# Kernel tuning notes

Measured on AMD Instinct MI355X. Metric: run time of the kernel, lower is better.

The kernel has to match this reference:

```python
import jax, jax.numpy as jnp
import numpy as np

B, CIN, COUT, KH, KW = 8, 64, 128, 3, 3
H = W = 64
STRIDE, PAD = 1, 1
G = 1  # deformable groups


def setup_inputs() -> dict:
    key = jax.random.key(0)
    k1, k2, k3 = jax.random.split(key, 3)
    rgb = jax.random.normal(k1, (B, CIN, H, W), dtype=jnp.float32)
    # torchvision layout: [B, 2*G*KH*KW, Ho, Wo], (dy, dx) pairs per kernel tap
    offsets = jax.random.normal(k2, (B, 2 * G * KH * KW, H, W), dtype=jnp.float32)
    # xavier_uniform for weight [COUT, CIN, KH, KW]
    fan_in, fan_out = CIN * KH * KW, COUT * KH * KW
    a = float(np.sqrt(6.0 / (fan_in + fan_out)))
    weight = jax.random.uniform(k3, (COUT, CIN, KH, KW), dtype=jnp.float32, minval=-a, maxval=a)
    bias = jnp.zeros((COUT,), dtype=jnp.float32)
    return {"rgb": rgb, "offsets": offsets, "weight": weight, "bias": bias}


def _deform_conv2d(rgb, offsets, weight, bias):
    b, cin, h, w = rgb.shape
    cout, _, kh, kw = weight.shape
    K = kh * kw
    ho = (h + 2 * PAD - kh) // STRIDE + 1
    wo = (w + 2 * PAD - kw) // STRIDE + 1
    cg = cin // G  # channels per deformable group

    off = offsets.reshape(b, G, K, 2, ho, wo)
    dy, dx = off[:, :, :, 0], off[:, :, :, 1]  # [b, G, K, ho, wo]

    ky, kx = jnp.meshgrid(jnp.arange(kh), jnp.arange(kw), indexing="ij")
    ky = ky.reshape(K).astype(jnp.float32)
    kx = kx.reshape(K).astype(jnp.float32)
    base_y = (jnp.arange(ho) * STRIDE - PAD).astype(jnp.float32)
    base_x = (jnp.arange(wo) * STRIDE - PAD).astype(jnp.float32)

    # sampling coordinates: p0 + kernel tap + learned offset -> [b, G, K, ho, wo]
    y = base_y[None, None, None, :, None] + ky[None, None, :, None, None] + dy
    x = base_x[None, None, None, None, :] + kx[None, None, :, None, None] + dx

    y0 = jnp.floor(y)
    x0 = jnp.floor(x)
    fy = y - y0
    fx = x - x0
    y0i = y0.astype(jnp.int32)
    x0i = x0.astype(jnp.int32)

    x_flat = rgb.reshape(b, G, cg, h * w)
    P = K * ho * wo

    def gather_corner(yc, xc, wgt):
        valid = (yc >= 0) & (yc < h) & (xc >= 0) & (xc < w)
        idx = jnp.clip(yc, 0, h - 1) * w + jnp.clip(xc, 0, w - 1)
        wgt = jnp.where(valid, wgt, 0.0).reshape(b, G, 1, P)
        vals = jnp.take_along_axis(x_flat, idx.reshape(b, G, 1, P), axis=3)
        return vals * wgt

    col = (
        gather_corner(y0i, x0i, (1 - fy) * (1 - fx))
        + gather_corner(y0i, x0i + 1, (1 - fy) * fx)
        + gather_corner(y0i + 1, x0i, fy * (1 - fx))
        + gather_corner(y0i + 1, x0i + 1, fy * fx)
    )  # [b, G, cg, K*ho*wo]

    col = col.reshape(b, cin * K, ho * wo)
    out = jnp.einsum("ok,bkp->bop", weight.reshape(cout, cin * K), col)
    return out.reshape(b, cout, ho, wo) + bias[None, :, None, None]


def reference(rgb, offsets, weight, bias):
    return _deform_conv2d(rgb, offsets, weight, bias)
```

## Files before the change

### kernel.cpp

```cpp
#include <hip/hip_runtime.h>

#define COUT_  128
#define KP     1024
#define CAPR   20
#define IMGC   (21 * 64)
#define IMGBUF (4 * IMGC)
#define COLU   36
#define COLBUF (64 * COLU)
#define WS_NEED (size_t)(COUT_ * KP * 2 + 8ull * 64 * 64 * 64 * 4)

#if __has_builtin(__builtin_amdgcn_fdot2_f32_bf16)
#define HAS_DOT2 1
#else
#define HAS_DOT2 0
#endif

typedef __attribute__((ext_vector_type(8))) __bf16 bf16x8;
typedef __attribute__((ext_vector_type(2))) __bf16 bf16x2;
typedef unsigned short u16x8 __attribute__((ext_vector_type(8)));
typedef __attribute__((ext_vector_type(4))) float f32x4;

__device__ __forceinline__ unsigned int f2bf(float f) {
    union { float f; unsigned int u; } c; c.f = f;
    unsigned int u = c.u;
    u += 0x7fffu + ((u >> 16) & 1u);
    return u >> 16;
}
__device__ __forceinline__ float bitsf(unsigned int u) {
    union { unsigned int u; float f; } c; c.u = u; return c.f;
}
__device__ __forceinline__ unsigned int pk2bf(float lo, float hi) {
    return f2bf(lo) | (f2bf(hi) << 16);
}
__device__ __forceinline__ bf16x2 mk_bf2(float lo, float hi) {
    unsigned int u = pk2bf(lo, hi);
    return __builtin_bit_cast(bf16x2, u);
}
__device__ __forceinline__ void gl_lds16(const unsigned int* g, unsigned int* l) {
    __builtin_amdgcn_global_load_lds(
        (const __attribute__((address_space(1))) unsigned int*)g,
        (__attribute__((address_space(3))) unsigned int*)l, 16, 0, 0);
}

__global__ void prep_weight(const float* __restrict__ w, unsigned short* __restrict__ wbf) {
    int idx = blockIdx.x * 256 + threadIdx.x;
    if (idx >= COUT_ * KP) return;
    int cout = idx >> 10, r = idx & 1023;
    int quad = r >> 6, j2 = r & 63;
    int k = j2 >> 2, j = j2 & 3;
    unsigned short v = 0;
    if (k < 9) {
        int cin = quad * 4 + j;
        v = (unsigned short)f2bf(w[(cout * 64 + cin) * 9 + k]);
    }
    wbf[idx] = v;
}

__global__ void prep_rgb(const float* __restrict__ rgb, unsigned int* __restrict__ rgbp) {
    int idx = blockIdx.x * 256 + threadIdx.x;
    float a = rgb[idx];
    float nb = ((idx & 63) == 63) ? 0.f : rgb[idx + 1];
    rgbp[idx] = f2bf(a) | (f2bf(nb) << 16);
}

template<bool PREP>
__launch_bounds__(256, 2)
__global__ void deform_mfma6(const float* __restrict__ rgb,
                             const unsigned int* __restrict__ rgbp,
                             const float* __restrict__ off,
                             const unsigned short* __restrict__ wbf,
                             const float* __restrict__ bias,
                             float* __restrict__ out) {
    __shared__ unsigned int S[2 * COLBUF + 2 * IMGBUF];
    __shared__ int sYmin, sYmax;
    unsigned int* imgU = S + 2 * COLBUF;

    const int t    = threadIdx.x;
    const int bid  = blockIdx.x;
    const int b    = bid & 7;
    const int ho   = bid >> 3;
    const int lane = t & 63;
    const int wv   = t >> 6;
    const int px   = lane;
    const int ln15 = lane & 15;
    const int q    = lane >> 4;

    const float* offb = off + b * (2 * 9 * 4096);

    {
        uint4* S4 = (uint4*)S;
        for (int i = t; i < (2 * COLBUF + 2 * IMGBUF) / 4; i += 256)
            S4[i] = make_uint4(0, 0, 0, 0);
    }
    if (t == 0) { sYmin = 64; sYmax = -1; }
    __syncthreads();

    float m_fy[3], m_fx[3]; int m_y0[3], m_x0[3];
    int lmin = 64, lmax = -1;
#pragma unroll
    for (int ti = 0; ti < 3; ti++) {
        const int kt = (ti < 2) ? (wv + ti * 4) : 8;
        const float dy = offb[((2 * kt)     * 64 + ho) * 64 + px];
        const float dx = offb[((2 * kt + 1) * 64 + ho) * 64 + px];
        const float y = (float)(ho - 1 + kt / 3) + dy;
        const float x = (float)(px - 1 + kt % 3) + dx;
        const float y0f = floorf(y), x0f = floorf(x);
        m_fy[ti] = y - y0f; m_fx[ti] = x - x0f;
        m_y0[ti] = (int)y0f; m_x0[ti] = (int)x0f;
        const int r0 = min(max(m_y0[ti], 0), 63), r1 = min(max(m_y0[ti] + 1, 0), 63);
        lmin = min(lmin, r0); lmax = max(lmax, r1);
    }
    atomicMin(&sYmin, lmin); atomicMax(&sYmax, lmax);
    __syncthreads();
    const int ymin  = sYmin;
    const int nrows = sYmax - ymin + 1;
    const int nr4   = min((nrows + 3) & ~3, CAPR);
    const int ymin2 = max(0, min(ymin, 64 - nr4));

    float4 sv[5];
    auto stage_dma = [&](int gg) {
        const unsigned int* gp = rgbp + ((unsigned)(b * 64 + gg * 4 + wv) * 64 + ymin2) * 64 + lane * 4;
        unsigned int* lp = imgU + (gg & 1) * IMGBUF + wv * IMGC;
        for (int r4 = 0; r4 < nr4; r4 += 4) gl_lds16(gp + r4 * 64, lp + r4 * 64);
    };
    auto stage_load = [&](int gg) {
        const float* gp = rgb + ((unsigned)(b * 64 + gg * 4 + wv) * 64 + ymin2 + (lane >> 4)) * 64 + (lane & 15) * 4;
        int n = 0;
        for (int r4 = 0; r4 < nr4; r4 += 4, n++) sv[n] = *(const float4*)(gp + r4 * 64);
    };
    auto stage_write = [&](int gg) {
        unsigned int* lp = imgU + (gg & 1) * IMGBUF + wv * IMGC + (lane >> 4) * 64 + (lane & 15) * 4;
        int n = 0;
        for (int r4 = 0; r4 < nr4; r4 += 4, n++) {
            const float4 v = sv[n];
            unsigned int b0 = f2bf(v.x), b1 = f2bf(v.y), b2 = f2bf(v.z), b3 = f2bf(v.w);
            unsigned int nb = __shfl(b0, lane + 1);
            if ((lane & 15) == 15) nb = 0;
            uint4 pk;
            pk.x = b0 | (b1 << 16); pk.y = b1 | (b2 << 16);
            pk.z = b2 | (b3 << 16); pk.w = b3 | (nb << 16);
            *(uint4*)(lp + r4 * 64) = pk;
        }
    };

    int ma[3];
#if HAS_DOT2
    bf16x2 wtp[3], wbp[3];
#else
    float mw[3][4];
#endif
#pragma unroll
    for (int ti = 0; ti < 3; ti++) {
        const int y0 = m_y0[ti], x0 = m_x0[ti];
        const float fy = m_fy[ti], fx = m_fx[ti];
        const int r0 = y0 - ymin2;
        const float wy0 = (y0 >= 0  && y0 < 64) ? (1.f - fy) : 0.f;
        const float wy1 = (y0 >= -1 && y0 < 63) ? fy         : 0.f;
        const bool ylo = (r0 < 0);
        const float wtop = ylo ? wy1 : wy0;
        const float wbot = ylo ? 0.f : wy1;
        const int r0c = ylo ? 0 : min(r0, nr4 - 1);
        const float wx0 = (x0 >= 0  && x0 < 64) ? (1.f - fx) : 0.f;
        const float wx1 = (x0 >= -1 && x0 < 63) ? fx         : 0.f;
        const bool xlo = (x0 < 0);
        const float wA = xlo ? wx1 : wx0;
        const float wB = xlo ? 0.f : wx1;
        const int xc = min(max(x0, 0), 63);
        ma[ti] = r0c * 64 + xc;
#if HAS_DOT2
        wtp[ti] = mk_bf2(wtop * wA, wtop * wB);
        wbp[ti] = mk_bf2(wbot * wA, wbot * wB);
#else
        mw[ti][0] = wtop * wA; mw[ti][1] = wtop * wB;
        mw[ti][2] = wbot * wA; mw[ti][3] = wbot * wB;
#endif
    }

    f32x4 acc[2][4] = {};
    const unsigned short* wrow0 = wbf + (wv * 32 + ln15) * KP;
    const unsigned short* wrow1 = wrow0 + 16 * KP;
    const unsigned short* col16 = (const unsigned short*)S;

    auto interp1 = [&](const unsigned int* pl, int ti) -> float {
        const unsigned int* p = pl + ma[ti];
        const unsigned int tp = p[0];
        const unsigned int bp = p[64];
#if HAS_DOT2
        float r = __builtin_amdgcn_fdot2_f32_bf16(__builtin_bit_cast(bf16x2, tp), wtp[ti], 0.f, false);
        return  __builtin_amdgcn_fdot2_f32_bf16(__builtin_bit_cast(bf16x2, bp), wbp[ti], r, false);
#else
        return mw[ti][0] * bitsf(tp << 16) + mw[ti][1] * bitsf(tp & 0xffff0000u)
             + mw[ti][2] * bitsf(bp << 16) + mw[ti][3] * bitsf(bp & 0xffff0000u);
#endif
    };
    auto gather = [&](int g) {
        const unsigned int* ib = imgU + (g & 1) * IMGBUF;
        unsigned int* cb = S + (g & 1) * COLBUF + px * COLU;
#pragma unroll
        for (int ti = 0; ti < 2; ti++) {
            const int kt = wv + ti * 4;
            uint2 w2;
            w2.x = pk2bf(interp1(ib, ti),            interp1(ib + IMGC, ti));
            w2.y = pk2bf(interp1(ib + 2 * IMGC, ti), interp1(ib + 3 * IMGC, ti));
            *(uint2*)&cb[kt * 2] = w2;
        }
        if (wv == (g & 3))
            cb[16] = pk2bf(interp1(ib, 2),            interp1(ib + IMGC, 2));
        if (wv == ((g + 2) & 3))
            cb[17] = pk2bf(interp1(ib + 2 * IMGC, 2), interp1(ib + 3 * IMGC, 2));
    };
    auto mfma_steps = [&](int gg) {
#pragma unroll
        for (int sg = 0; sg < 2; sg++) {
            const int s = 2 * gg + sg;
            const u16x8 a0u = *(const u16x8*)(wrow0 + s * 32 + q * 8);
            const u16x8 a1u = *(const u16x8*)(wrow1 + s * 32 + q * 8);
            const bf16x8 a0 = __builtin_bit_cast(bf16x8, a0u);
            const bf16x8 a1 = __builtin_bit_cast(bf16x8, a1u);
#pragma unroll
            for (int nj = 0; nj < 4; nj++) {
                const u16x8 bu = *(const u16x8*)(col16 + (gg & 1) * (COLBUF * 2)
                                                 + (nj * 16 + ln15) * (COLU * 2) + sg * 32 + q * 8);
                const bf16x8 bv = __builtin_bit_cast(bf16x8, bu);
                acc[0][nj] = __builtin_amdgcn_mfma_f32_16x16x32_bf16(a0, bv, acc[0][nj], 0, 0, 0);
                acc[1][nj] = __builtin_amdgcn_mfma_f32_16x16x32_bf16(a1, bv, acc[1][nj], 0, 0, 0);
            }
        }
    };

    if (PREP) stage_dma(0); else stage_load(0);
    if (!PREP) stage_write(0);
    __syncthreads();

    for (int g = 0; g < 16; g++) {
        if (g + 1 < 16) { if (PREP) stage_dma(g + 1); else stage_load(g + 1); }
        if (g > 0) mfma_steps(g - 1);
        gather(g);
        if (!PREP && g + 1 < 16) stage_write(g + 1);
        __syncthreads();
    }
    mfma_steps(15);

#pragma unroll
    for (int mi = 0; mi < 2; mi++) {
#pragma unroll
        for (int r = 0; r < 4; r++) {
            const int cout = wv * 32 + mi * 16 + q * 4 + r;
            const float bv = bias[cout];
            float* orow = out + ((b * COUT_ + cout) * 64 + ho) * 64;
#pragma unroll
            for (int nj = 0; nj < 4; nj++)
                orow[nj * 16 + ln15] = acc[mi][nj][r] + bv;
        }
    }
}

extern "C" void kernel_launch(void* const* d_in, const int* in_sizes, int n_in,
                              void* d_out, int out_size, void* d_ws, size_t ws_size,
                              hipStream_t stream) {
    const float* rgb  = (const float*)d_in[0];
    const float* off  = (const float*)d_in[1];
    const float* w    = (const float*)d_in[2];
    const float* bias = (const float*)d_in[3];
    float* out = (float*)d_out;
    unsigned short* wbf = (unsigned short*)d_ws;
    unsigned int* rgbp  = (unsigned int*)((char*)d_ws + COUT_ * KP * 2);

    prep_weight<<<(COUT_ * KP + 255) / 256, 256, 0, stream>>>(w, wbf);
    if (ws_size >= WS_NEED) {
        prep_rgb<<<8 * 64 * 4096 / 256, 256, 0, stream>>>(rgb, rgbp);
        deform_mfma6<true><<<512, 256, 0, stream>>>(rgb, rgbp, off, wbf, bias, out);
    } else {
        deform_mfma6<false><<<512, 256, 0, stream>>>(rgb, nullptr, off, wbf, bias, out);
    }
}
```

Baseline: 107.6 us.

## Split output rows into half-width tiles, fuse prep kernels, smaller per-step channel groups

Each block now covers 32 output pixels of a row instead of 64, doubling the grid to 1024 blocks and raising launch bounds to 4 blocks per CU. The smaller LDS footprint comes from processing two channels per step over 32 steps with a reduced row cap. The weight layout is repacked for two-channel groups, and the weight A-fragments are prefetched one step ahead. The two prep kernels are merged into one launch. The change aims at better occupancy and fewer launches, but it adds twice as many barriers per block and duplicates offset and staging work across the half-row tiles.

```diff
diff --git a/kernel.cpp b/kernel.cpp
--- a/kernel.cpp
+++ b/kernel.cpp
@@ -2,11 +2,11 @@
 
 #define COUT_  128
 #define KP     1024
-#define CAPR   20
-#define IMGC   (21 * 64)
-#define IMGBUF (4 * IMGC)
-#define COLU   36
-#define COLBUF (64 * COLU)
+#define CAPR   16
+#define IMGP   (17 * 64)
+#define IMGBUF (2 * IMGP)
+#define COLW   20
+#define COLBUF (32 * COLW)
 #define WS_NEED (size_t)(COUT_ * KP * 2 + 8ull * 64 * 64 * 64 * 4)
 
 #if __has_builtin(__builtin_amdgcn_fdot2_f32_bf16)
@@ -42,30 +42,29 @@
         (__attribute__((address_space(3))) unsigned int*)l, 16, 0, 0);
 }
 
-__global__ void prep_weight(const float* __restrict__ w, unsigned short* __restrict__ wbf) {
-    int idx = blockIdx.x * 256 + threadIdx.x;
-    if (idx >= COUT_ * KP) return;
-    int cout = idx >> 10, r = idx & 1023;
-    int quad = r >> 6, j2 = r & 63;
-    int k = j2 >> 2, j = j2 & 3;
-    unsigned short v = 0;
-    if (k < 9) {
-        int cin = quad * 4 + j;
-        v = (unsigned short)f2bf(w[(cout * 64 + cin) * 9 + k]);
-    }
-    wbf[idx] = v;
-}
-
-__global__ void prep_rgb(const float* __restrict__ rgb, unsigned int* __restrict__ rgbp) {
-    int idx = blockIdx.x * 256 + threadIdx.x;
-    float a = rgb[idx];
-    float nb = ((idx & 63) == 63) ? 0.f : rgb[idx + 1];
-    rgbp[idx] = f2bf(a) | (f2bf(nb) << 16);
+__global__ void prep_all(const float* __restrict__ w, unsigned short* __restrict__ wbf,
+                         const float* __restrict__ rgb, unsigned int* __restrict__ rgbp,
+                         int do_rgb) {
+    const int bx = blockIdx.x;
+    if (bx < 512) {
+        int idx = bx * 256 + threadIdx.x;
+        int cout = idx >> 10, r = idx & 1023;
+        int pair = r >> 5, j2 = r & 31;
+        int k = j2 >> 1, par = j2 & 1;
+        unsigned short v = 0;
+        if (j2 < 18) v = (unsigned short)f2bf(w[(cout * 64 + pair * 2 + par) * 9 + k]);
+        wbf[idx] = v;
+    } else if (do_rgb) {
+        int idx = (bx - 512) * 256 + threadIdx.x;
+        float a = rgb[idx];
+        float nb = ((idx & 63) == 63) ? 0.f : rgb[idx + 1];
+        rgbp[idx] = f2bf(a) | (f2bf(nb) << 16);
+    }
 }
 
 template<bool PREP>
-__launch_bounds__(256, 2)
-__global__ void deform_mfma6(const float* __restrict__ rgb,
+__launch_bounds__(256, 4)
+__global__ void deform_mfma9(const float* __restrict__ rgb,
                              const unsigned int* __restrict__ rgbp,
                              const float* __restrict__ off,
                              const unsigned short* __restrict__ wbf,
@@ -78,10 +77,12 @@
     const int t    = threadIdx.x;
     const int bid  = blockIdx.x;
     const int b    = bid & 7;
-    const int ho   = bid >> 3;
+    const int ho   = (bid >> 3) & 63;
+    const int px0  = (bid >> 9) * 32;
     const int lane = t & 63;
     const int wv   = t >> 6;
-    const int px   = lane;
+    const int px   = t & 31;
+    const int tg   = t >> 5;
     const int ln15 = lane & 15;
     const int q    = lane >> 4;
 
@@ -89,21 +90,22 @@
 
     {
         uint4* S4 = (uint4*)S;
-        for (int i = t; i < (2 * COLBUF + 2 * IMGBUF) / 4; i += 256)
-            S4[i] = make_uint4(0, 0, 0, 0);
+        const int n4 = (2 * COLBUF + 2 * IMGBUF) / 4;
+        for (int i = t; i < n4; i += 256) S4[i] = make_uint4(0, 0, 0, 0);
     }
     if (t == 0) { sYmin = 64; sYmax = -1; }
     __syncthreads();
 
-    float m_fy[3], m_fx[3]; int m_y0[3], m_x0[3];
+    float m_fy[2], m_fx[2]; int m_y0[2], m_x0[2];
     int lmin = 64, lmax = -1;
 #pragma unroll
-    for (int ti = 0; ti < 3; ti++) {
-        const int kt = (ti < 2) ? (wv + ti * 4) : 8;
-        const float dy = offb[((2 * kt)     * 64 + ho) * 64 + px];
-        const float dx = offb[((2 * kt + 1) * 64 + ho) * 64 + px];
+    for (int ti = 0; ti < 2; ti++) {
+        const int kt = ti ? 8 : tg;
+        const int wo = px0 + px;
+        const float dy = offb[((2 * kt)     * 64 + ho) * 64 + wo];
+        const float dx = offb[((2 * kt + 1) * 64 + ho) * 64 + wo];
         const float y = (float)(ho - 1 + kt / 3) + dy;
-        const float x = (float)(px - 1 + kt % 3) + dx;
+        const float x = (float)(wo - 1 + kt % 3) + dx;
         const float y0f = floorf(y), x0f = floorf(x);
         m_fy[ti] = y - y0f; m_fx[ti] = x - x0f;
         m_y0[ti] = (int)y0f; m_x0[ti] = (int)x0f;
@@ -117,40 +119,58 @@
     const int nr4   = min((nrows + 3) & ~3, CAPR);
     const int ymin2 = max(0, min(ymin, 64 - nr4));
 
-    float4 sv[5];
     auto stage_dma = [&](int gg) {
-        const unsigned int* gp = rgbp + ((unsigned)(b * 64 + gg * 4 + wv) * 64 + ymin2) * 64 + lane * 4;
-        unsigned int* lp = imgU + (gg & 1) * IMGBUF + wv * IMGC;
-        for (int r4 = 0; r4 < nr4; r4 += 4) gl_lds16(gp + r4 * 64, lp + r4 * 64);
-    };
+#pragma unroll
+        for (int u = 0; u < 2; u++) {
+            const int c = wv + u * 4;
+            const int plane = c >> 2, r4 = (c & 3) * 4;
+            if (r4 < nr4) {
+                const unsigned int* gp = rgbp
+                    + ((unsigned)(b * 64 + gg * 2 + plane) * 64 + ymin2 + r4) * 64 + lane * 4;
+                unsigned int* lp = imgU + (gg & 1) * IMGBUF + plane * IMGP + r4 * 64;
+                gl_lds16(gp, lp);
+            }
+        }
+    };
+    float4 sv[2];
     auto stage_load = [&](int gg) {
-        const float* gp = rgb + ((unsigned)(b * 64 + gg * 4 + wv) * 64 + ymin2 + (lane >> 4)) * 64 + (lane & 15) * 4;
-        int n = 0;
-        for (int r4 = 0; r4 < nr4; r4 += 4, n++) sv[n] = *(const float4*)(gp + r4 * 64);
+#pragma unroll
+        for (int u = 0; u < 2; u++) {
+            const int c = wv + u * 4;
+            const int plane = c >> 2, r4 = (c & 3) * 4;
+            if (r4 < nr4)
+                sv[u] = *(const float4*)(rgb
+                    + ((unsigned)(b * 64 + gg * 2 + plane) * 64 + ymin2 + r4 + (lane >> 4)) * 64
+                    + (lane & 15) * 4);
+        }
     };
     auto stage_write = [&](int gg) {
-        unsigned int* lp = imgU + (gg & 1) * IMGBUF + wv * IMGC + (lane >> 4) * 64 + (lane & 15) * 4;
-        int n = 0;
-        for (int r4 = 0; r4 < nr4; r4 += 4, n++) {
-            const float4 v = sv[n];
+#pragma unroll
+        for (int u = 0; u < 2; u++) {
+            const int c = wv + u * 4;
+            const int plane = c >> 2, r4 = (c & 3) * 4;
+            const float4 v = sv[u];
             unsigned int b0 = f2bf(v.x), b1 = f2bf(v.y), b2 = f2bf(v.z), b3 = f2bf(v.w);
             unsigned int nb = __shfl(b0, lane + 1);
             if ((lane & 15) == 15) nb = 0;
-            uint4 pk;
-            pk.x = b0 | (b1 << 16); pk.y = b1 | (b2 << 16);
-            pk.z = b2 | (b3 << 16); pk.w = b3 | (nb << 16);
-            *(uint4*)(lp + r4 * 64) = pk;
-        }
-    };
-
-    int ma[3];
+            if (r4 < nr4) {
+                uint4 pk;
+                pk.x = b0 | (b1 << 16); pk.y = b1 | (b2 << 16);
+                pk.z = b2 | (b3 << 16); pk.w = b3 | (nb << 16);
+                *(uint4*)(imgU + (gg & 1) * IMGBUF + plane * IMGP
+                          + (r4 + (lane >> 4)) * 64 + (lane & 15) * 4) = pk;
+            }
+        }
+    };
+
+    int ma[2];
 #if HAS_DOT2
-    bf16x2 wtp[3], wbp[3];
-#else
-    float mw[3][4];
-#endif
-#pragma unroll
-    for (int ti = 0; ti < 3; ti++) {
+    bf16x2 wtp[2], wbp[2];
+#else
+    float mw[2][4];
+#endif
+#pragma unroll
+    for (int ti = 0; ti < 2; ti++) {
         const int y0 = m_y0[ti], x0 = m_x0[ti];
         const float fy = m_fy[ti], fx = m_fx[ti];
         const int r0 = y0 - ymin2;
@@ -176,7 +196,7 @@
 #endif
     }
 
-    f32x4 acc[2][4] = {};
+    f32x4 acc[2][2] = {};
     const unsigned short* wrow0 = wbf + (wv * 32 + ln15) * KP;
     const unsigned short* wrow1 = wrow0 + 16 * KP;
     const unsigned short* col16 = (const unsigned short*)S;
@@ -195,51 +215,39 @@
     };
     auto gather = [&](int g) {
         const unsigned int* ib = imgU + (g & 1) * IMGBUF;
-        unsigned int* cb = S + (g & 1) * COLBUF + px * COLU;
-#pragma unroll
-        for (int ti = 0; ti < 2; ti++) {
-            const int kt = wv + ti * 4;
-            uint2 w2;
-            w2.x = pk2bf(interp1(ib, ti),            interp1(ib + IMGC, ti));
-            w2.y = pk2bf(interp1(ib + 2 * IMGC, ti), interp1(ib + 3 * IMGC, ti));
-            *(uint2*)&cb[kt * 2] = w2;
-        }
-        if (wv == (g & 3))
-            cb[16] = pk2bf(interp1(ib, 2),            interp1(ib + IMGC, 2));
-        if (wv == ((g + 2) & 3))
-            cb[17] = pk2bf(interp1(ib + 2 * IMGC, 2), interp1(ib + 3 * IMGC, 2));
-    };
-    auto mfma_steps = [&](int gg) {
-#pragma unroll
-        for (int sg = 0; sg < 2; sg++) {
-            const int s = 2 * gg + sg;
-            const u16x8 a0u = *(const u16x8*)(wrow0 + s * 32 + q * 8);
-            const u16x8 a1u = *(const u16x8*)(wrow1 + s * 32 + q * 8);
-            const bf16x8 a0 = __builtin_bit_cast(bf16x8, a0u);
-            const bf16x8 a1 = __builtin_bit_cast(bf16x8, a1u);
-#pragma unroll
-            for (int nj = 0; nj < 4; nj++) {
-                const u16x8 bu = *(const u16x8*)(col16 + (gg & 1) * (COLBUF * 2)
-                                                 + (nj * 16 + ln15) * (COLU * 2) + sg * 32 + q * 8);
-                const bf16x8 bv = __builtin_bit_cast(bf16x8, bu);
-                acc[0][nj] = __builtin_amdgcn_mfma_f32_16x16x32_bf16(a0, bv, acc[0][nj], 0, 0, 0);
-                acc[1][nj] = __builtin_amdgcn_mfma_f32_16x16x32_bf16(a1, bv, acc[1][nj], 0, 0, 0);
-            }
-        }
-    };
-
-    if (PREP) stage_dma(0); else stage_load(0);
-    if (!PREP) stage_write(0);
+        unsigned int* cb = S + (g & 1) * COLBUF + px * COLW;
+        cb[tg] = pk2bf(interp1(ib, 0), interp1(ib + IMGP, 0));
+        if (tg == (g & 7))
+            cb[8] = pk2bf(interp1(ib, 1), interp1(ib + IMGP, 1));
+    };
+    auto mfma_step = [&](int g, u16x8 a0u, u16x8 a1u) {
+        const bf16x8 a0 = __builtin_bit_cast(bf16x8, a0u);
+        const bf16x8 a1 = __builtin_bit_cast(bf16x8, a1u);
+        const unsigned short* cp = col16 + (g & 1) * (COLBUF * 2) + q * 8;
+#pragma unroll
+        for (int nj = 0; nj < 2; nj++) {
+            const u16x8 bu = *(const u16x8*)(cp + (nj * 16 + ln15) * (COLW * 2));
+            const bf16x8 bv = __builtin_bit_cast(bf16x8, bu);
+            acc[0][nj] = __builtin_amdgcn_mfma_f32_16x16x32_bf16(a0, bv, acc[0][nj], 0, 0, 0);
+            acc[1][nj] = __builtin_amdgcn_mfma_f32_16x16x32_bf16(a1, bv, acc[1][nj], 0, 0, 0);
+        }
+    };
+
+    if (PREP) stage_dma(0); else { stage_load(0); stage_write(0); }
     __syncthreads();
 
-    for (int g = 0; g < 16; g++) {
-        if (g + 1 < 16) { if (PREP) stage_dma(g + 1); else stage_load(g + 1); }
-        if (g > 0) mfma_steps(g - 1);
+    u16x8 pA0 = {}, pA1 = {};
+    for (int g = 0; g < 32; g++) {
+        if (g + 1 < 32) { if (PREP) stage_dma(g + 1); else stage_load(g + 1); }
+        u16x8 nA0 = *(const u16x8*)(wrow0 + g * 32 + q * 8);
+        u16x8 nA1 = *(const u16x8*)(wrow1 + g * 32 + q * 8);
+        if (g > 0) mfma_step(g - 1, pA0, pA1);
         gather(g);
-        if (!PREP && g + 1 < 16) stage_write(g + 1);
+        if (!PREP && g + 1 < 32) stage_write(g + 1);
         __syncthreads();
-    }
-    mfma_steps(15);
+        pA0 = nA0; pA1 = nA1;
+    }
+    mfma_step(31, pA0, pA1);
 
 #pragma unroll
     for (int mi = 0; mi < 2; mi++) {
@@ -247,9 +255,9 @@
         for (int r = 0; r < 4; r++) {
             const int cout = wv * 32 + mi * 16 + q * 4 + r;
             const float bv = bias[cout];
-            float* orow = out + ((b * COUT_ + cout) * 64 + ho) * 64;
-#pragma unroll
-            for (int nj = 0; nj < 4; nj++)
+            float* orow = out + ((b * COUT_ + cout) * 64 + ho) * 64 + px0;
+#pragma unroll
+            for (int nj = 0; nj < 2; nj++)
                 orow[nj * 16 + ln15] = acc[mi][nj][r] + bv;
         }
     }
@@ -266,11 +274,10 @@
     unsigned short* wbf = (unsigned short*)d_ws;
     unsigned int* rgbp  = (unsigned int*)((char*)d_ws + COUT_ * KP * 2);
 
-    prep_weight<<<(COUT_ * KP + 255) / 256, 256, 0, stream>>>(w, wbf);
-    if (ws_size >= WS_NEED) {
-        prep_rgb<<<8 * 64 * 4096 / 256, 256, 0, stream>>>(rgb, rgbp);
-        deform_mfma6<true><<<512, 256, 0, stream>>>(rgb, rgbp, off, wbf, bias, out);
-    } else {
-        deform_mfma6<false><<<512, 256, 0, stream>>>(rgb, nullptr, off, wbf, bias, out);
-    }
-}
+    const int do_rgb = (ws_size >= WS_NEED) ? 1 : 0;
+    prep_all<<<do_rgb ? 8704 : 512, 256, 0, stream>>>(w, wbf, rgb, rgbp, do_rgb);
+    if (do_rgb)
+        deform_mfma9<true><<<1024, 256, 0, stream>>>(rgb, rgbp, off, wbf, bias, out);
+    else
+        deform_mfma9<false><<<1024, 256, 0, stream>>>(rgb, nullptr, off, wbf, bias, out);
+}
```

New measurement: 116.4 us. +8.1%, slower.
